# Optimization experiments

Hardware: AMD Instinct MI355X
Metric: run time of the kernel (lower is better)

## Reference

```python
import jax, jax.numpy as jnp
import numpy as np

B, T, H, NH = 4, 2048, 1024, 16
HD = H // NH  # 64


def setup_inputs() -> dict:
    key = jax.random.key(0)
    ks = jax.random.split(key, 8)
    s = 0.02
    return {
        "hidden_states": jax.random.normal(ks[0], (B, T, H), dtype=jnp.float32),
        "attention_mask": jnp.zeros((B, 1, 1, T), dtype=jnp.float32),
        "Wq": jax.random.normal(ks[1], (H, H), dtype=jnp.float32) * s,
        "bq": jnp.zeros((H,), dtype=jnp.float32),
        "Wk": jax.random.normal(ks[2], (H, H), dtype=jnp.float32) * s,
        "bk": jnp.zeros((H,), dtype=jnp.float32),
        "Wv": jax.random.normal(ks[3], (H, H), dtype=jnp.float32) * s,
        "bv": jnp.zeros((H,), dtype=jnp.float32),
    }


def _split_heads(x):
    # [B, T, H] -> [B, NH, T, HD]
    b, t, _ = x.shape
    return x.reshape(b, t, NH, HD).transpose(0, 2, 1, 3)


def reference(hidden_states, attention_mask, Wq, bq, Wk, bk, Wv, bv):
    # QKV projections (torch Linear: x @ W.T + b)
    q = _split_heads(hidden_states @ Wq.T + bq)
    k = _split_heads(hidden_states @ Wk.T + bk)
    v = _split_heads(hidden_states @ Wv.T + bv)

    scale = HD ** (-0.5)
    # [B, NH, T, T]
    scores = jnp.einsum("bhqd,bhkd->bhqk", q, k) * scale
    t = q.shape[2]
    causal = jnp.triu(jnp.ones((t, t), dtype=bool), k=1)
    scores = jnp.where(causal[None, None], -jnp.inf, scores)
    scores = scores + attention_mask  # additive mask [B,1,1,T]
    probs = jax.nn.softmax(scores, axis=-1)
    # dropout is identity in eval mode
    out = jnp.einsum("bhqk,bhkd->bhqd", probs, v)
    # [B, NH, T, HD] -> [B, T, H]
    return out.transpose(0, 2, 1, 3).reshape(hidden_states.shape[0], t, H)
```

## Files before the change

### kernel.cpp

```cpp
#include <hip/hip_runtime.h>
#include <math.h>

#define B_  4
#define T_  2048
#define H_  1024
#define NH_ 16
#define HD_ 64

typedef __bf16  bf16x8  __attribute__((ext_vector_type(8)));
typedef float   f32x4   __attribute__((ext_vector_type(4)));
typedef unsigned short ushort8v __attribute__((ext_vector_type(8)));
typedef short   short4v __attribute__((ext_vector_type(4)));

__device__ __forceinline__ unsigned short f2bf(float f) {
    unsigned int u = __builtin_bit_cast(unsigned int, f);
    u += 0x7fffu + ((u >> 16) & 1u);
    return (unsigned short)(u >> 16);
}

__device__ __forceinline__ f32x4 mfma16x16x16bf16(short4v a, short4v b, f32x4 c) {
#if __has_builtin(__builtin_amdgcn_mfma_f32_16x16x16bf16_1k)
    return __builtin_amdgcn_mfma_f32_16x16x16bf16_1k(a, b, c, 0, 0, 0);
#else
    f32x4 d = c;
    asm volatile("v_mfma_f32_16x16x16_bf16 %0, %1, %2, %0\n\ts_nop 7\n\ts_nop 7"
                 : "+v"(d) : "v"(a), "v"(b));
    return d;
#endif
}

__device__ __forceinline__ void gload_lds16(const unsigned short* g,
                                            unsigned short* l) {
    __builtin_amdgcn_global_load_lds(
        (const __attribute__((address_space(1))) unsigned int*)g,
        (__attribute__((address_space(3))) unsigned int*)l, 16, 0, 0);
}

#define SBARRIER()   asm volatile("s_barrier" ::: "memory")
#define LGKMCNT0()   asm volatile("s_waitcnt lgkmcnt(0)" ::: "memory")
#define VMCNT6()     asm volatile("s_waitcnt vmcnt(6)" ::: "memory")
#define VMCNT0()     asm volatile("s_waitcnt vmcnt(0)" ::: "memory")

__global__ void cvt_all(const float* __restrict__ hs,
                        const float* __restrict__ Wq,
                        const float* __restrict__ Wk,
                        const float* __restrict__ Wv,
                        unsigned short* __restrict__ Xo,
                        unsigned short* __restrict__ oq,
                        unsigned short* __restrict__ ok,
                        unsigned short* __restrict__ ov) {
    const int bid = blockIdx.x;
    const float* in;
    unsigned short* out;
    int i;
    if (bid < 4096) {
        in = hs; out = Xo; i = bid * 256 + threadIdx.x;
    } else {
        const int r = bid - 4096;
        const int z = r >> 9;
        in  = (z == 0) ? Wq : (z == 1) ? Wk : Wv;
        out = (z == 0) ? oq : (z == 1) ? ok : ov;
        i = (r & 511) * 256 + threadIdx.x;
    }
    const float4* p = reinterpret_cast<const float4*>(in) + (size_t)i * 2;
    float4 f0 = p[0], f1 = p[1];
    ushort8v o;
    o[0] = f2bf(f0.x); o[1] = f2bf(f0.y); o[2] = f2bf(f0.z); o[3] = f2bf(f0.w);
    o[4] = f2bf(f1.x); o[5] = f2bf(f1.y); o[6] = f2bf(f1.z); o[7] = f2bf(f1.w);
    reinterpret_cast<ushort8v*>(out)[i] = o;
}

__global__ __launch_bounds__(512) void qkv_gemm_all(
    const unsigned short* __restrict__ X,
    const unsigned short* __restrict__ Wq,
    const unsigned short* __restrict__ Wk,
    const unsigned short* __restrict__ Wv,
    const float* __restrict__ bq,
    const float* __restrict__ bk,
    const float* __restrict__ bv,
    unsigned short* __restrict__ Qo,
    unsigned short* __restrict__ Ko,
    unsigned short* __restrict__ Vo)
{
    const int id     = blockIdx.x;
    const int xcd    = id & 7;
    const int within = id >> 3;
    const int z      = within >> 5;
    const int rest   = within & 31;
    const int xb     = rest & 7;
    const int yb     = xcd * 4 + (rest >> 3);

    const unsigned short* W = (z == 0) ? Wq : (z == 1) ? Wk : Wv;
    const float* bias = (z == 0) ? bq : (z == 1) ? bk : bv;
    unsigned short* out = (z == 0) ? Qo : (z == 1) ? Ko : Vo;

    const int K = 1024;
    const int t    = threadIdx.x;
    const int lane = t & 63;
    const int wid  = t >> 6;
    const int lo = lane & 15, hi = lane >> 4;
    const int wm = wid >> 1, wn = wid & 1;
    const int m0 = yb * 256;
    const int n0 = xb * 128;

    __shared__ unsigned short As[2][256 * 64];
    __shared__ unsigned short Bs[2][128 * 64];

    const int srowoff = lane >> 3;
    const int scol    = lane & 7;

    f32x4 acc[4][4];
#pragma unroll
    for (int i = 0; i < 4; ++i)
#pragma unroll
        for (int j = 0; j < 4; ++j) acc[i][j] = (f32x4){0.f, 0.f, 0.f, 0.f};

#define STAGE_(AS, BS, KOFF)                                                  \
    do {                                                                      \
        _Pragma("unroll") for (int p = 0; p < 4; ++p) {                       \
            const int rowb = p * 64 + wid * 8;                                \
            const int row  = rowb + srowoff;                                  \
            const int c16  = scol ^ (row & 7);                                \
            gload_lds16(&X[(size_t)(m0 + row) * K + (KOFF) + c16 * 8],        \
                        &(AS)[rowb * 64]);                                    \
        }                                                                     \
        _Pragma("unroll") for (int p = 0; p < 2; ++p) {                       \
            const int rowb = p * 64 + wid * 8;                                \
            const int row  = rowb + srowoff;                                  \
            const int c16  = scol ^ (row & 7);                                \
            gload_lds16(&W[(size_t)(n0 + row) * K + (KOFF) + c16 * 8],        \
                        &(BS)[rowb * 64]);                                    \
        }                                                                     \
    } while (0)

#define KTILE_(AS, BS, HAVE_NEXT, KOFF_NEXT)                                  \
    do {                                                                      \
        bf16x8 a[4][2], bfr[4][2];                                            \
        _Pragma("unroll") for (int mt = 0; mt < 4; ++mt)                      \
            _Pragma("unroll") for (int ks = 0; ks < 2; ++ks)                  \
                a[mt][ks] = *reinterpret_cast<const bf16x8*>(                 \
                    &(AS)[(wm * 64 + mt * 16 + lo) * 64 +                     \
                          (((ks * 4 + hi) ^ (lo & 7)) * 8)]);                 \
        _Pragma("unroll") for (int nt = 0; nt < 4; ++nt)                      \
            _Pragma("unroll") for (int ks = 0; ks < 2; ++ks)                  \
                bfr[nt][ks] = *reinterpret_cast<const bf16x8*>(               \
                    &(BS)[(wn * 64 + nt * 16 + lo) * 64 +                     \
                          (((ks * 4 + hi) ^ (lo & 7)) * 8)]);                 \
        LGKMCNT0();                                                           \
        SBARRIER();                                                           \
        if (HAVE_NEXT) STAGE_(AS, BS, KOFF_NEXT);                             \
        __builtin_amdgcn_s_setprio(1);                                        \
        _Pragma("unroll") for (int mt = 0; mt < 4; ++mt)                      \
            _Pragma("unroll") for (int nt = 0; nt < 4; ++nt)                  \
                acc[mt][nt] = __builtin_amdgcn_mfma_f32_16x16x32_bf16(        \
                    a[mt][0], bfr[nt][0], acc[mt][nt], 0, 0, 0);              \
        _Pragma("unroll") for (int mt = 0; mt < 4; ++mt)                      \
            _Pragma("unroll") for (int nt = 0; nt < 4; ++nt)                  \
                acc[mt][nt] = __builtin_amdgcn_mfma_f32_16x16x32_bf16(        \
                    a[mt][1], bfr[nt][1], acc[mt][nt], 0, 0, 0);              \
        __builtin_amdgcn_s_setprio(0);                                        \
        if (HAVE_NEXT) VMCNT6(); else VMCNT0();                               \
        SBARRIER();                                                           \
    } while (0)

    STAGE_(As[0], Bs[0], 0);
    STAGE_(As[1], Bs[1], 64);
    VMCNT6();
    SBARRIER();

#pragma unroll
    for (int k0 = 0; k0 < K; k0 += 128) {
        KTILE_(As[0], Bs[0], (k0 + 128 < K), k0 + 128);
        KTILE_(As[1], Bs[1], (k0 + 192 < K), k0 + 192);
    }

#pragma unroll
    for (int nt = 0; nt < 4; ++nt) {
        int n = n0 + wn * 64 + nt * 16 + lo;
        float bv_ = bias[n];
        int h = n >> 6, d = n & 63;
#pragma unroll
        for (int mt = 0; mt < 4; ++mt) {
            int mbase = m0 + wm * 64 + mt * 16 + hi * 4;
            int bb = mbase >> 11;
            int tt = mbase & 2047;
            int ct = (tt >> 4) & 3;
            size_t tilebase = ((size_t)(bb * NH_ + h) * 32 + (tt >> 6)) * 4096;
            if (z == 2) {
                ushort4 pk;
                pk.x = f2bf(acc[mt][nt][0] + bv_);
                pk.y = f2bf(acc[mt][nt][1] + bv_);
                pk.z = f2bf(acc[mt][nt][2] + bv_);
                pk.w = f2bf(acc[mt][nt][3] + bv_);
                *reinterpret_cast<ushort4*>(
                    &out[tilebase + (size_t)ct * 1024 + (size_t)(hi * 16 + lo) * 16 + nt * 4]) = pk;
            } else if (z == 1) {
                const int ksd = d >> 5;
                const int hif = (d >> 3) & 3;
                const int jd  = d & 7;
                size_t fragbase = tilebase + (size_t)(ct * 2 + ksd) * 512;
#pragma unroll
                for (int r = 0; r < 4; ++r)
                    out[fragbase + (size_t)(hif * 16 + hi * 4 + r) * 8 + jd] =
                        f2bf(acc[mt][nt][r] + bv_);
            } else {
                size_t base = (size_t)(bb * NH_ + h) * T_;
#pragma unroll
                for (int r = 0; r < 4; ++r)
                    out[(base + tt + r) * HD_ + d] = f2bf(acc[mt][nt][r] + bv_);
            }
        }
    }
#undef STAGE_
#undef KTILE_
}

__global__ __launch_bounds__(128, 2) void attn_fwd15(
    const unsigned short* __restrict__ Q,
    const unsigned short* __restrict__ Kf,
    const unsigned short* __restrict__ Vf,
    const float* __restrict__ amask,
    float* __restrict__ out)
{
    const float SC    = 0.125f * 1.44269504089f;
    const float LOG2E = 1.44269504089f;

    const int lane = threadIdx.x & 63;
    const int w    = threadIdx.x >> 6;
    const int lo = lane & 15, hi = lane >> 4;

    const int bid    = blockIdx.x;
    const int xcd    = bid & 7;
    const int within = bid >> 3;
    const int bh     = xcd * 8 + (within & 7);
    const int u      = 63 - (within >> 3);
    const int b      = bh >> 4;
    const int h      = bh & 15;

    const unsigned short* Qg = Q + (size_t)bh * T_ * HD_;
    const float* am = amask + (size_t)b * T_;
    float* outBase = out + (size_t)b * T_ * H_ + h * HD_;

    __shared__ f32x4 Lo[2][4][64];
    __shared__ float Ll[2][64];

    const int q0   = u * 32;
    const int nt   = (u >> 1) + 1;
    const int half = nt >> 1;
    const int ktBeg = w ? half : 0;
    const int ktEnd = w ? nt : half;

    bf16x8 qf[2][2];
#pragma unroll
    for (int mt = 0; mt < 2; ++mt)
#pragma unroll
        for (int ks = 0; ks < 2; ++ks)
            qf[mt][ks] = *reinterpret_cast<const bf16x8*>(
                &Qg[(size_t)(q0 + mt * 16 + lo) * HD_ + ks * 32 + hi * 8]);

    f32x4 o[2][4];
#pragma unroll
    for (int mt = 0; mt < 2; ++mt)
#pragma unroll
        for (int dt = 0; dt < 4; ++dt) o[mt][dt] = (f32x4){0.f, 0.f, 0.f, 0.f};
    float l_r[2] = {0.f, 0.f};

    const unsigned short* kp = Kf + ((size_t)bh * 32 + ktBeg) * 4096;
    const unsigned short* vp = Vf + ((size_t)bh * 32 + ktBeg) * 4096;
    const float*          ap = am + ktBeg * 64;

    for (int kt = ktBeg; kt < ktEnd; ++kt, kp += 4096, vp += 4096, ap += 64) {
        const int kv0 = kt * 64;

        bf16x8 kf[4][2];
#pragma unroll
        for (int ct = 0; ct < 4; ++ct)
#pragma unroll
            for (int ks = 0; ks < 2; ++ks)
                kf[ct][ks] = *reinterpret_cast<const bf16x8*>(
                    &kp[(ct * 2 + ks) * 512 + lane * 8]);

        short4v vf[4][4];
#pragma unroll
        for (int ct = 0; ct < 4; ++ct) {
            union { ushort8v u8; short4v s4[2]; } va, vb;
            va.u8 = *reinterpret_cast<const ushort8v*>(&vp[ct * 1024 + lane * 16]);
            vb.u8 = *reinterpret_cast<const ushort8v*>(&vp[ct * 1024 + lane * 16 + 8]);
            vf[0][ct] = va.s4[0];
            vf[1][ct] = va.s4[1];
            vf[2][ct] = vb.s4[0];
            vf[3][ct] = vb.s4[1];
        }

        f32x4 amv[4];
#pragma unroll
        for (int ct = 0; ct < 4; ++ct)
            amv[ct] = *reinterpret_cast<const f32x4*>(&ap[ct * 16 + hi * 4]) * LOG2E;

        f32x4 s[2][4];
#pragma unroll
        for (int mt = 0; mt < 2; ++mt)
#pragma unroll
            for (int ct = 0; ct < 4; ++ct) s[mt][ct] = (f32x4){0.f, 0.f, 0.f, 0.f};
#pragma unroll
        for (int ks = 0; ks < 2; ++ks)
#pragma unroll
            for (int ct = 0; ct < 4; ++ct)
#pragma unroll
                for (int mt = 0; mt < 2; ++mt)
                    s[mt][ct] = __builtin_amdgcn_mfma_f32_16x16x32_bf16(
                        kf[ct][ks], qf[mt][ks], s[mt][ct], 0, 0, 0);

        const bool edge = (kv0 + 63 > q0);

        short4v p[2][4];
#pragma unroll
        for (int mt = 0; mt < 2; ++mt) {
            f32x4 rsv = (f32x4){0.f, 0.f, 0.f, 0.f};
#pragma unroll
            for (int ct = 0; ct < 4; ++ct) {
                f32x4 sv;
#pragma unroll
                for (int r = 0; r < 4; ++r)
                    sv[r] = fmaf(s[mt][ct][r], SC, amv[ct][r]);
                if (edge) {
                    const int q = q0 + mt * 16 + lo;
#pragma unroll
                    for (int r = 0; r < 4; ++r)
                        if (kv0 + ct * 16 + hi * 4 + r > q) sv[r] = -INFINITY;
                }
                short4v pk;
#pragma unroll
                for (int r = 0; r < 4; ++r) {
                    float pe = exp2f(sv[r]);
                    rsv[r] += pe;
                    __bf16 hb = (__bf16)pe;
                    pk[r] = __builtin_bit_cast(short, hb);
                }
                p[mt][ct] = pk;
            }
            l_r[mt] += (rsv[0] + rsv[1]) + (rsv[2] + rsv[3]);
        }

#pragma unroll
        for (int ct = 0; ct < 4; ++ct)
#pragma unroll
            for (int mt = 0; mt < 2; ++mt)
#pragma unroll
                for (int dt = 0; dt < 4; ++dt)
                    o[mt][dt] = mfma16x16x16bf16(vf[dt][ct], p[mt][ct], o[mt][dt]);
    }

    if (w == 1) {
#pragma unroll
        for (int mt = 0; mt < 2; ++mt) {
            Ll[mt][lane] = l_r[mt];
#pragma unroll
            for (int dt = 0; dt < 4; ++dt)
                Lo[mt][dt][lane] = o[mt][dt];
        }
    }
    __syncthreads();
    if (w == 0) {
#pragma unroll
        for (int mt = 0; mt < 2; ++mt) {
            float lf = l_r[mt] + Ll[mt][lane];
            lf += __shfl_xor(lf, 16, 64);
            lf += __shfl_xor(lf, 32, 64);
            const float inv = 1.0f / lf;
            const int tq = q0 + mt * 16 + lo;
            float* orow = outBase + (size_t)tq * H_;
#pragma unroll
            for (int dt = 0; dt < 4; ++dt) {
                f32x4 v = (o[mt][dt] + Lo[mt][dt][lane]) * inv;
                *reinterpret_cast<f32x4*>(&orow[dt * 16 + hi * 4]) = v;
            }
        }
    }
}

extern "C" void kernel_launch(void* const* d_in, const int* in_sizes, int n_in,
                              void* d_out, int out_size, void* d_ws, size_t ws_size,
                              hipStream_t stream) {
    const float* hs    = (const float*)d_in[0];
    const float* amask = (const float*)d_in[1];
    const float* Wq    = (const float*)d_in[2];
    const float* bq    = (const float*)d_in[3];
    const float* Wk    = (const float*)d_in[4];
    const float* bk    = (const float*)d_in[5];
    const float* Wv    = (const float*)d_in[6];
    const float* bv    = (const float*)d_in[7];
    float* out = (float*)d_out;

    unsigned short* Xbf = (unsigned short*)d_ws;
    unsigned short* Wqb = Xbf + (size_t)8192 * 1024;
    unsigned short* Wkb = Wqb + (size_t)1024 * 1024;
    unsigned short* Wvb = Wkb + (size_t)1024 * 1024;
    unsigned short* Qb  = Wvb + (size_t)1024 * 1024;
    unsigned short* Kfb = Qb  + (size_t)B_ * NH_ * T_ * HD_;
    unsigned short* Vfb = Kfb + (size_t)B_ * NH_ * T_ * HD_;

    cvt_all<<<5632, 256, 0, stream>>>(hs, Wq, Wk, Wv, Xbf, Wqb, Wkb, Wvb);

    qkv_gemm_all<<<768, 512, 0, stream>>>(Xbf, Wqb, Wkb, Wvb, bq, bk, bv,
                                          Qb, Kfb, Vfb);

    attn_fwd15<<<4096, 128, 0, stream>>>(Qb, Kfb, Vfb, amask, out);
}
```

Measured before the change: 152.1 us.

## Triple-buffer QKV projection GEMM LDS staging with split half-tile fragment loads

The QKV projection GEMM goes from double-buffered to triple-buffered LDS staging, so global-to-LDS loads are issued three k-tiles ahead with matching vmcnt waits. Each k-tile is also split into two halves: fragments for the first k-substep are read and issued to MFMA before the second half's fragments are loaded, which lowers register pressure. The goal is to hide more global memory latency. In exchange it raises LDS use to 144KB per block, which may limit occupancy, and adds an extra barrier per k-tile.

New measurement: 155.0 us. About the same (+1.9%).

```diff
diff --git a/kernel.cpp b/kernel.cpp
--- a/kernel.cpp
+++ b/kernel.cpp
@@ -38,6 +38,7 @@
 
 #define SBARRIER()   asm volatile("s_barrier" ::: "memory")
 #define LGKMCNT0()   asm volatile("s_waitcnt lgkmcnt(0)" ::: "memory")
+#define VMCNT12()    asm volatile("s_waitcnt vmcnt(12)" ::: "memory")
 #define VMCNT6()     asm volatile("s_waitcnt vmcnt(6)" ::: "memory")
 #define VMCNT0()     asm volatile("s_waitcnt vmcnt(0)" ::: "memory")
 
@@ -103,8 +104,8 @@
     const int m0 = yb * 256;
     const int n0 = xb * 128;
 
-    __shared__ unsigned short As[2][256 * 64];
-    __shared__ unsigned short Bs[2][128 * 64];
+    __shared__ unsigned short As[3][256 * 64];
+    __shared__ unsigned short Bs[3][128 * 64];
 
     const int srowoff = lane >> 3;
     const int scol    = lane & 7;
@@ -133,45 +134,62 @@
         }                                                                     \
     } while (0)
 
-#define KTILE_(AS, BS, HAVE_NEXT, KOFF_NEXT)                                  \
-    do {                                                                      \
-        bf16x8 a[4][2], bfr[4][2];                                            \
-        _Pragma("unroll") for (int mt = 0; mt < 4; ++mt)                      \
-            _Pragma("unroll") for (int ks = 0; ks < 2; ++ks)                  \
-                a[mt][ks] = *reinterpret_cast<const bf16x8*>(                 \
-                    &(AS)[(wm * 64 + mt * 16 + lo) * 64 +                     \
-                          (((ks * 4 + hi) ^ (lo & 7)) * 8)]);                 \
-        _Pragma("unroll") for (int nt = 0; nt < 4; ++nt)                      \
-            _Pragma("unroll") for (int ks = 0; ks < 2; ++ks)                  \
-                bfr[nt][ks] = *reinterpret_cast<const bf16x8*>(               \
-                    &(BS)[(wn * 64 + nt * 16 + lo) * 64 +                     \
-                          (((ks * 4 + hi) ^ (lo & 7)) * 8)]);                 \
-        LGKMCNT0();                                                           \
-        SBARRIER();                                                           \
-        if (HAVE_NEXT) STAGE_(AS, BS, KOFF_NEXT);                             \
-        __builtin_amdgcn_s_setprio(1);                                        \
-        _Pragma("unroll") for (int mt = 0; mt < 4; ++mt)                      \
-            _Pragma("unroll") for (int nt = 0; nt < 4; ++nt)                  \
-                acc[mt][nt] = __builtin_amdgcn_mfma_f32_16x16x32_bf16(        \
-                    a[mt][0], bfr[nt][0], acc[mt][nt], 0, 0, 0);              \
-        _Pragma("unroll") for (int mt = 0; mt < 4; ++mt)                      \
-            _Pragma("unroll") for (int nt = 0; nt < 4; ++nt)                  \
-                acc[mt][nt] = __builtin_amdgcn_mfma_f32_16x16x32_bf16(        \
-                    a[mt][1], bfr[nt][1], acc[mt][nt], 0, 0, 0);              \
-        __builtin_amdgcn_s_setprio(0);                                        \
-        if (HAVE_NEXT) VMCNT6(); else VMCNT0();                               \
-        SBARRIER();                                                           \
-    } while (0)
-
     STAGE_(As[0], Bs[0], 0);
     STAGE_(As[1], Bs[1], 64);
-    VMCNT6();
+    STAGE_(As[2], Bs[2], 128);
+    VMCNT12();
     SBARRIER();
 
 #pragma unroll
-    for (int k0 = 0; k0 < K; k0 += 128) {
-        KTILE_(As[0], Bs[0], (k0 + 128 < K), k0 + 128);
-        KTILE_(As[1], Bs[1], (k0 + 192 < K), k0 + 192);
+    for (int kt = 0; kt < 16; ++kt) {
+        unsigned short* Abuf = As[kt % 3];
+        unsigned short* Bbuf = Bs[kt % 3];
+
+        bf16x8 a0[4], b0[4];
+#pragma unroll
+        for (int mt = 0; mt < 4; ++mt)
+            a0[mt] = *reinterpret_cast<const bf16x8*>(
+                &Abuf[(wm * 64 + mt * 16 + lo) * 64 + ((hi ^ (lo & 7)) * 8)]);
+#pragma unroll
+        for (int nt = 0; nt < 4; ++nt)
+            b0[nt] = *reinterpret_cast<const bf16x8*>(
+                &Bbuf[(wn * 64 + nt * 16 + lo) * 64 + ((hi ^ (lo & 7)) * 8)]);
+        LGKMCNT0();
+        SBARRIER();
+        __builtin_amdgcn_s_setprio(1);
+#pragma unroll
+        for (int mt = 0; mt < 4; ++mt)
+#pragma unroll
+            for (int nt = 0; nt < 4; ++nt)
+                acc[mt][nt] = __builtin_amdgcn_mfma_f32_16x16x32_bf16(
+                    a0[mt], b0[nt], acc[mt][nt], 0, 0, 0);
+        __builtin_amdgcn_s_setprio(0);
+
+        bf16x8 a1[4], b1[4];
+#pragma unroll
+        for (int mt = 0; mt < 4; ++mt)
+            a1[mt] = *reinterpret_cast<const bf16x8*>(
+                &Abuf[(wm * 64 + mt * 16 + lo) * 64 + (((4 + hi) ^ (lo & 7)) * 8)]);
+#pragma unroll
+        for (int nt = 0; nt < 4; ++nt)
+            b1[nt] = *reinterpret_cast<const bf16x8*>(
+                &Bbuf[(wn * 64 + nt * 16 + lo) * 64 + (((4 + hi) ^ (lo & 7)) * 8)]);
+        LGKMCNT0();
+        SBARRIER();
+        if (kt + 3 < 16) STAGE_(Abuf, Bbuf, (kt + 3) * 64);
+        __builtin_amdgcn_s_setprio(1);
+#pragma unroll
+        for (int mt = 0; mt < 4; ++mt)
+#pragma unroll
+            for (int nt = 0; nt < 4; ++nt)
+                acc[mt][nt] = __builtin_amdgcn_mfma_f32_16x16x32_bf16(
+                    a1[mt], b1[nt], acc[mt][nt], 0, 0, 0);
+        __builtin_amdgcn_s_setprio(0);
+
+        if (kt + 3 < 16)      VMCNT12();
+        else if (kt + 2 < 16) VMCNT6();
+        else if (kt + 1 < 16) VMCNT0();
+        SBARRIER();
     }
 
 #pragma unroll
@@ -212,7 +230,6 @@
         }
     }
 #undef STAGE_
-#undef KTILE_
 }
 
 __global__ __launch_bounds__(128, 2) void attn_fwd15(
```

## Pre-swizzle weights into MFMA fragment layout and load B operands directly to registers

Applied to the files above, without the earlier changes.

The weight conversion kernel now writes the bf16 weights in a per-lane MFMA fragment order instead of row-major. The QKV GEMM then reads its B operands straight from global memory into double-buffered registers, dropping the B tile from LDS and its LDS reads. The A tile still streams through LDS, and the vmcnt waits are retuned to the new mix of outstanding loads. This saves LDS capacity and bandwidth, at the cost of more live registers and B loads that are not shared between waves, which relies on L2/L1 for reuse.

Result: slower. 161.0 us (+5.9%).

```diff
diff --git a/kernel.cpp b/kernel.cpp
--- a/kernel.cpp
+++ b/kernel.cpp
@@ -38,7 +38,8 @@
 
 #define SBARRIER()   asm volatile("s_barrier" ::: "memory")
 #define LGKMCNT0()   asm volatile("s_waitcnt lgkmcnt(0)" ::: "memory")
-#define VMCNT6()     asm volatile("s_waitcnt vmcnt(6)" ::: "memory")
+#define VMCNT12()    asm volatile("s_waitcnt vmcnt(12)" ::: "memory")
+#define VMCNT8()     asm volatile("s_waitcnt vmcnt(8)" ::: "memory")
 #define VMCNT0()     asm volatile("s_waitcnt vmcnt(0)" ::: "memory")
 
 __global__ void cvt_all(const float* __restrict__ hs,
@@ -50,31 +51,40 @@
                         unsigned short* __restrict__ ok,
                         unsigned short* __restrict__ ov) {
     const int bid = blockIdx.x;
-    const float* in;
-    unsigned short* out;
-    int i;
     if (bid < 4096) {
-        in = hs; out = Xo; i = bid * 256 + threadIdx.x;
+        const int i = bid * 256 + threadIdx.x;
+        const float4* p = reinterpret_cast<const float4*>(hs) + (size_t)i * 2;
+        float4 f0 = p[0], f1 = p[1];
+        ushort8v o;
+        o[0] = f2bf(f0.x); o[1] = f2bf(f0.y); o[2] = f2bf(f0.z); o[3] = f2bf(f0.w);
+        o[4] = f2bf(f1.x); o[5] = f2bf(f1.y); o[6] = f2bf(f1.z); o[7] = f2bf(f1.w);
+        reinterpret_cast<ushort8v*>(Xo)[i] = o;
     } else {
         const int r = bid - 4096;
         const int z = r >> 9;
-        in  = (z == 0) ? Wq : (z == 1) ? Wk : Wv;
-        out = (z == 0) ? oq : (z == 1) ? ok : ov;
-        i = (r & 511) * 256 + threadIdx.x;
-    }
-    const float4* p = reinterpret_cast<const float4*>(in) + (size_t)i * 2;
-    float4 f0 = p[0], f1 = p[1];
-    ushort8v o;
-    o[0] = f2bf(f0.x); o[1] = f2bf(f0.y); o[2] = f2bf(f0.z); o[3] = f2bf(f0.w);
-    o[4] = f2bf(f1.x); o[5] = f2bf(f1.y); o[6] = f2bf(f1.z); o[7] = f2bf(f1.w);
-    reinterpret_cast<ushort8v*>(out)[i] = o;
+        const float* in = (z == 0) ? Wq : (z == 1) ? Wk : Wv;
+        unsigned short* out = (z == 0) ? oq : (z == 1) ? ok : ov;
+        const int i = (r & 511) * 256 + threadIdx.x;
+        const int n  = i >> 7;
+        const int kb = (i & 127) * 8;
+        const float4* p = reinterpret_cast<const float4*>(in) + (size_t)i * 2;
+        float4 f0 = p[0], f1 = p[1];
+        ushort8v o;
+        o[0] = f2bf(f0.x); o[1] = f2bf(f0.y); o[2] = f2bf(f0.z); o[3] = f2bf(f0.w);
+        o[4] = f2bf(f1.x); o[5] = f2bf(f1.y); o[6] = f2bf(f1.z); o[7] = f2bf(f1.w);
+        const int nb = n >> 7, wn = (n >> 6) & 1, nt = (n >> 4) & 3, lo = n & 15;
+        const int kt = kb >> 6, ks = (kb >> 5) & 1, hi = (kb >> 3) & 3;
+        const int lane = hi * 16 + lo;
+        size_t off = (((((size_t)(nb * 16 + kt) * 2 + wn) * 4 + nt) * 2 + ks) * 64 + lane) * 8;
+        *reinterpret_cast<ushort8v*>(&out[off]) = o;
+    }
 }
 
 __global__ __launch_bounds__(512) void qkv_gemm_all(
     const unsigned short* __restrict__ X,
-    const unsigned short* __restrict__ Wq,
-    const unsigned short* __restrict__ Wk,
-    const unsigned short* __restrict__ Wv,
+    const unsigned short* __restrict__ Wqf,
+    const unsigned short* __restrict__ Wkf,
+    const unsigned short* __restrict__ Wvf,
     const float* __restrict__ bq,
     const float* __restrict__ bk,
     const float* __restrict__ bv,
@@ -90,7 +100,7 @@
     const int xb     = rest & 7;
     const int yb     = xcd * 4 + (rest >> 3);
 
-    const unsigned short* W = (z == 0) ? Wq : (z == 1) ? Wk : Wv;
+    const unsigned short* Wf = (z == 0) ? Wqf : (z == 1) ? Wkf : Wvf;
     const float* bias = (z == 0) ? bq : (z == 1) ? bk : bv;
     unsigned short* out = (z == 0) ? Qo : (z == 1) ? Ko : Vo;
 
@@ -101,10 +111,10 @@
     const int lo = lane & 15, hi = lane >> 4;
     const int wm = wid >> 1, wn = wid & 1;
     const int m0 = yb * 256;
-    const int n0 = xb * 128;
+
+    const unsigned short* Wb = Wf + (size_t)xb * 131072;
 
     __shared__ unsigned short As[2][256 * 64];
-    __shared__ unsigned short Bs[2][128 * 64];
 
     const int srowoff = lane >> 3;
     const int scol    = lane & 7;
@@ -115,7 +125,7 @@
 #pragma unroll
         for (int j = 0; j < 4; ++j) acc[i][j] = (f32x4){0.f, 0.f, 0.f, 0.f};
 
-#define STAGE_(AS, BS, KOFF)                                                  \
+#define STAGEA_(AS, KOFF)                                                     \
     do {                                                                      \
         _Pragma("unroll") for (int p = 0; p < 4; ++p) {                       \
             const int rowb = p * 64 + wid * 8;                                \
@@ -124,59 +134,62 @@
             gload_lds16(&X[(size_t)(m0 + row) * K + (KOFF) + c16 * 8],        \
                         &(AS)[rowb * 64]);                                    \
         }                                                                     \
-        _Pragma("unroll") for (int p = 0; p < 2; ++p) {                       \
-            const int rowb = p * 64 + wid * 8;                                \
-            const int row  = rowb + srowoff;                                  \
-            const int c16  = scol ^ (row & 7);                                \
-            gload_lds16(&W[(size_t)(n0 + row) * K + (KOFF) + c16 * 8],        \
-                        &(BS)[rowb * 64]);                                    \
-        }                                                                     \
     } while (0)
 
-#define KTILE_(AS, BS, HAVE_NEXT, KOFF_NEXT)                                  \
+#define BLOAD_(BR, KT)                                                        \
     do {                                                                      \
-        bf16x8 a[4][2], bfr[4][2];                                            \
+        _Pragma("unroll") for (int nt = 0; nt < 4; ++nt)                      \
+            _Pragma("unroll") for (int ks = 0; ks < 2; ++ks)                  \
+                BR[nt][ks] = *reinterpret_cast<const bf16x8*>(                \
+                    &Wb[(size_t)((((KT) * 2 + wn) * 4 + nt) * 2 + ks) * 512   \
+                        + lane * 8]);                                         \
+    } while (0)
+
+#define KTILE_(AS, BCUR, BNXT, KT)                                            \
+    do {                                                                      \
+        bf16x8 a[4][2];                                                       \
         _Pragma("unroll") for (int mt = 0; mt < 4; ++mt)                      \
             _Pragma("unroll") for (int ks = 0; ks < 2; ++ks)                  \
                 a[mt][ks] = *reinterpret_cast<const bf16x8*>(                 \
                     &(AS)[(wm * 64 + mt * 16 + lo) * 64 +                     \
                           (((ks * 4 + hi) ^ (lo & 7)) * 8)]);                 \
-        _Pragma("unroll") for (int nt = 0; nt < 4; ++nt)                      \
-            _Pragma("unroll") for (int ks = 0; ks < 2; ++ks)                  \
-                bfr[nt][ks] = *reinterpret_cast<const bf16x8*>(               \
-                    &(BS)[(wn * 64 + nt * 16 + lo) * 64 +                     \
-                          (((ks * 4 + hi) ^ (lo & 7)) * 8)]);                 \
         LGKMCNT0();                                                           \
-        SBARRIER();                                                           \
-        if (HAVE_NEXT) STAGE_(AS, BS, KOFF_NEXT);                             \
+        SBARRIER();                         \
+        if ((KT) + 2 < 16) STAGEA_(AS, ((KT) + 2) * 64);         \
+        if ((KT) + 1 < 16) BLOAD_(BNXT, (KT) + 1);               \
+        if ((KT) + 2 < 16)      { VMCNT12(); }                                \
+        else if ((KT) + 1 < 16) { VMCNT8();  }                                \
+        else                    { VMCNT0();  }                                \
         __builtin_amdgcn_s_setprio(1);                                        \
         _Pragma("unroll") for (int mt = 0; mt < 4; ++mt)                      \
             _Pragma("unroll") for (int nt = 0; nt < 4; ++nt)                  \
                 acc[mt][nt] = __builtin_amdgcn_mfma_f32_16x16x32_bf16(        \
-                    a[mt][0], bfr[nt][0], acc[mt][nt], 0, 0, 0);              \
+                    a[mt][0], BCUR[nt][0], acc[mt][nt], 0, 0, 0);             \
         _Pragma("unroll") for (int mt = 0; mt < 4; ++mt)                      \
             _Pragma("unroll") for (int nt = 0; nt < 4; ++nt)                  \
                 acc[mt][nt] = __builtin_amdgcn_mfma_f32_16x16x32_bf16(        \
-                    a[mt][1], bfr[nt][1], acc[mt][nt], 0, 0, 0);              \
+                    a[mt][1], BCUR[nt][1], acc[mt][nt], 0, 0, 0);             \
         __builtin_amdgcn_s_setprio(0);                                        \
-        if (HAVE_NEXT) VMCNT6(); else VMCNT0();                               \
-        SBARRIER();                                                           \
+        SBARRIER();                      \
     } while (0)
 
-    STAGE_(As[0], Bs[0], 0);
-    STAGE_(As[1], Bs[1], 64);
-    VMCNT6();
+    bf16x8 b0[4][2], b1[4][2];
+
+    STAGEA_(As[0], 0);
+    STAGEA_(As[1], 64);
+    BLOAD_(b0, 0);
+    VMCNT12();
     SBARRIER();
 
 #pragma unroll
-    for (int k0 = 0; k0 < K; k0 += 128) {
-        KTILE_(As[0], Bs[0], (k0 + 128 < K), k0 + 128);
-        KTILE_(As[1], Bs[1], (k0 + 192 < K), k0 + 192);
+    for (int kt = 0; kt < 16; kt += 2) {
+        KTILE_(As[0], b0, b1, kt);
+        KTILE_(As[1], b1, b0, kt + 1);
     }
 
 #pragma unroll
     for (int nt = 0; nt < 4; ++nt) {
-        int n = n0 + wn * 64 + nt * 16 + lo;
+        int n = xb * 128 + wn * 64 + nt * 16 + lo;
         float bv_ = bias[n];
         int h = n >> 6, d = n & 63;
 #pragma unroll
@@ -211,7 +224,8 @@
             }
         }
     }
-#undef STAGE_
+#undef STAGEA_
+#undef BLOAD_
 #undef KTILE_
 }
 
```
